# Optimization experiments

Measured on AMD Instinct MI355X. Metric: run time of the kernel, lower is better.

Reference implementation:

```python
import jax, jax.numpy as jnp
import numpy as np

N, E, G = 30000, 480000, 64
IN, H, L = 24, 512, 6


def setup_inputs() -> dict:
    key = jax.random.key(0)
    ks = jax.random.split(key, 20)
    s = 0.05
    inp = {
        "x": jax.random.normal(ks[0], (N, IN), dtype=jnp.float32),
        "edge_index": jax.random.randint(ks[1], (2, E), 0, N, dtype=jnp.int64),
        "batch": jnp.sort(jax.random.randint(ks[2], (N,), 0, G, dtype=jnp.int64)),
        # node encoder
        "enc_w": jax.random.normal(ks[3], (IN, H), dtype=jnp.float32) * s,
        "enc_b": jnp.zeros((H,), dtype=jnp.float32),
        # per-layer message MLP (stacked over L layers), weights stored [in, out]
        "mlp_w1": jax.random.normal(ks[4], (L, H, H), dtype=jnp.float32) * s,
        "mlp_b1": jnp.zeros((L, H), dtype=jnp.float32),
        "mlp_w2": jax.random.normal(ks[5], (L, H, H), dtype=jnp.float32) * s,
        "mlp_b2": jnp.zeros((L, H), dtype=jnp.float32),
        # per-layer GRUCell params, [in, 3H] layout (gates order: r, z, n)
        "gru_wih": jax.random.normal(ks[6], (L, H, 3 * H), dtype=jnp.float32) * s,
        "gru_whh": jax.random.normal(ks[7], (L, H, 3 * H), dtype=jnp.float32) * s,
        "gru_bih": jnp.zeros((L, 3 * H), dtype=jnp.float32),
        "gru_bhh": jnp.zeros((L, 3 * H), dtype=jnp.float32),
        # head MLP
        "head_w1": jax.random.normal(ks[8], (H, H // 2), dtype=jnp.float32) * s,
        "head_b1": jnp.zeros((H // 2,), dtype=jnp.float32),
        "head_w2": jax.random.normal(ks[9], (H // 2, 1), dtype=jnp.float32) * s,
        "head_b2": jnp.zeros((1,), dtype=jnp.float32),
    }
    return inp


def _forward(x, edge_index, batch, enc_w, enc_b, mlp_w1, mlp_b1, mlp_w2, mlp_b2,
             gru_wih, gru_whh, gru_bih, gru_bhh, head_w1, head_b1, head_w2, head_b2):
    src, dst = edge_index[0], edge_index[1]
    h = x @ enc_w + enc_b  # [N, H]
    for l in range(L):
        # message MLP depends only on x_j, so compute per-node then gather
        msg = jnp.maximum(h @ mlp_w1[l] + mlp_b1[l], 0.0) @ mlp_w2[l] + mlp_b2[l]  # [N, H]
        # scatter-add over edges + self-loop contribution (add_self_loops)
        m = jax.ops.segment_sum(msg[src], dst, num_segments=N) + msg  # [N, H]
        # GRUCell(input=m, hidden=h); torch gate order: reset, update, new
        gi = m @ gru_wih[l] + gru_bih[l]
        gh = h @ gru_whh[l] + gru_bhh[l]
        r = jax.nn.sigmoid(gi[:, :H] + gh[:, :H])
        z = jax.nn.sigmoid(gi[:, H:2 * H] + gh[:, H:2 * H])
        n = jnp.tanh(gi[:, 2 * H:] + r * gh[:, 2 * H:])
        h = (1.0 - z) * n + z * h
    # global mean pool per graph
    sums = jax.ops.segment_sum(h, batch, num_segments=G)
    cnt = jax.ops.segment_sum(jnp.ones((N,), dtype=h.dtype), batch, num_segments=G)
    pooled = sums / jnp.maximum(cnt, 1.0)[:, None]  # [G, H]
    out = jnp.maximum(pooled @ head_w1 + head_b1, 0.0) @ head_w2 + head_b2
    return out[:, 0]  # [G]


def reference(x, edge_index, batch, enc_w, enc_b, mlp_w1, mlp_b1, mlp_w2, mlp_b2,
              gru_wih, gru_whh, gru_bih, gru_bhh, head_w1, head_b1, head_w2, head_b2):
    return _forward(x, edge_index, batch, enc_w, enc_b, mlp_w1, mlp_b1, mlp_w2, mlp_b2,
                    gru_wih, gru_whh, gru_bih, gru_bhh, head_w1, head_b1, head_w2, head_b2)
```

## Files before the change

kernel.cpp:

```cpp
#include <hip/hip_runtime.h>
#include <hip/hip_bf16.h>
#include <math.h>

#define N_NODES 30000
#define N_EDGES 480000
#define N_GRAPH 64
#define DIN 24
#define HD 512
#define NL 6

typedef __hip_bfloat16 bf16;
using short8 = __attribute__((ext_vector_type(8))) short;
using f32x4 = __attribute__((ext_vector_type(4))) float;

#define ASYNC16(gp, lp)                                              \
    __builtin_amdgcn_global_load_lds(                                \
        (const __attribute__((address_space(1))) void*)(gp),         \
        (__attribute__((address_space(3))) void*)(lp), 16, 0, 0)

__device__ __forceinline__ float sigmoidf_(float x) { return 1.0f / (1.0f + expf(-x)); }
__device__ __forceinline__ float b2f(unsigned short u) {
    return __uint_as_float(((unsigned int)u) << 16);
}
__device__ __forceinline__ unsigned short f2b(float f) {
    bf16 b = __float2bfloat16(f);
    return *(unsigned short*)&b;
}

__global__ __launch_bounds__(256) void enc_kernel(const float* __restrict__ x,
                                                  const float* __restrict__ w,
                                                  const float* __restrict__ b,
                                                  bf16* __restrict__ h) {
    __shared__ float xs[DIN];
    int row = blockIdx.x;
    int tid = threadIdx.x;
    if (tid < DIN) xs[tid] = x[row * DIN + tid];
    __syncthreads();
    for (int c = tid; c < HD; c += 256) {
        float acc = b[c];
#pragma unroll
        for (int k = 0; k < DIN; k++) acc = fmaf(xs[k], w[k * HD + c], acc);
        h[(size_t)row * HD + c] = __float2bfloat16(acc);
    }
}

__global__ __launch_bounds__(256) void twcvt_kernel(const float* __restrict__ W,
                                                    bf16* __restrict__ WtH,
                                                    bf16* __restrict__ WtL, int Nc) {
    __shared__ float s[32][33];
    int l = blockIdx.z;
    const float* Wp = W + (size_t)l * HD * Nc;
    size_t ob = (size_t)l * HD * Nc;
    int k0 = blockIdx.y * 32, c0 = blockIdx.x * 32;
    int tx = threadIdx.x & 31, ty = threadIdx.x >> 5;
    for (int r = ty; r < 32; r += 8) s[r][tx] = Wp[(size_t)(k0 + r) * Nc + c0 + tx];
    __syncthreads();
    for (int r = ty; r < 32; r += 8) {
        float v = s[tx][r];
        unsigned short hu = f2b(v);
        float hf = b2f(hu);
        size_t o = ob + (size_t)(c0 + r) * HD + k0 + tx;
        *(unsigned short*)&WtH[o] = hu;
        WtL[o] = __float2bfloat16(v - hf);
    }
}

template <bool RELU>
__global__ __launch_bounds__(256) void gemm_mfma(const bf16* __restrict__ A,
                                                 const bf16* __restrict__ WtH,
                                                 const bf16* __restrict__ WtL,
                                                 const float* __restrict__ bias,
                                                 bf16* __restrict__ C, int n) {
    __shared__ bf16 As[128 * 32];
    __shared__ bf16 BH[128 * 32];
    __shared__ bf16 BL[128 * 32];
    int tid = threadIdx.x;
    int wv = tid >> 6, lane = tid & 63;
    int quad = lane >> 4, l16 = lane & 15;
    int crow = lane >> 2, cseg = lane & 3;
    int gseg = cseg ^ ((crow >> 1) & 3);
    int fsw = (quad ^ ((l16 >> 1) & 3)) * 8;
    int row0 = blockIdx.y * 128, col0 = blockIdx.x * 128;
    f32x4 acc[2][8] = {};

    int aoff[4], alds[4];
    int boff[8];
    const bf16* wb = (wv == 2) ? WtH : WtL;
    bf16* bdst = (wv == 2) ? BH : BL;
    if (wv < 2) {
#pragma unroll
        for (int j = 0; j < 4; j++) {
            int ch = wv * 4 + j;
            int gr = row0 + ch * 16 + crow;
            if (gr > n - 1) gr = n - 1;
            aoff[j] = gr * HD + gseg * 8;
            alds[j] = ch * 512;
        }
    } else {
#pragma unroll
        for (int s = 0; s < 8; s++) boff[s] = (col0 + s * 16 + crow) * HD + gseg * 8;
    }

    for (int kt = 0; kt < 512; kt += 32) {
        if (wv < 2) {
#pragma unroll
            for (int j = 0; j < 4; j++) ASYNC16(&A[aoff[j] + kt], &As[alds[j]]);
        } else {
#pragma unroll
            for (int s = 0; s < 8; s++) ASYNC16(&wb[boff[s] + kt], &bdst[s * 512]);
        }
        __syncthreads();
        short8 bhf[2], blf[2];
#pragma unroll
        for (int t = 0; t < 2; t++) {
            int fo = (wv * 32 + t * 16 + l16) * 32 + fsw;
            bhf[t] = *(const short8*)&BH[fo];
            blf[t] = *(const short8*)&BL[fo];
        }
#pragma unroll
        for (int i = 0; i < 8; i++) {
            short8 af = *(const short8*)&As[(i * 16 + l16) * 32 + fsw];
#pragma unroll
            for (int t = 0; t < 2; t++) {
                acc[t][i] = __builtin_amdgcn_mfma_f32_16x16x32_bf16(af, bhf[t], acc[t][i], 0, 0, 0);
                acc[t][i] = __builtin_amdgcn_mfma_f32_16x16x32_bf16(af, blf[t], acc[t][i], 0, 0, 0);
            }
        }
        __syncthreads();
    }
#pragma unroll
    for (int t = 0; t < 2; t++) {
        int col = col0 + wv * 32 + t * 16 + l16;
        float bb = bias[col];
#pragma unroll
        for (int i = 0; i < 8; i++) {
#pragma unroll
            for (int r = 0; r < 4; r++) {
                int row = row0 + i * 16 + quad * 4 + r;
                if (row < n) {
                    float v = acc[t][i][r] + bb;
                    if (RELU) v = fmaxf(v, 0.0f);
                    C[(size_t)row * HD + col] = __float2bfloat16(v);
                }
            }
        }
    }
}

__global__ __launch_bounds__(256, 2) void gru_mfma(const bf16* __restrict__ M,
                                                   const bf16* __restrict__ Hc,
                                                   const bf16* __restrict__ WiH,
                                                   const bf16* __restrict__ WiL,
                                                   const bf16* __restrict__ WhH,
                                                   const bf16* __restrict__ WhL,
                                                   const float* __restrict__ bih,
                                                   const float* __restrict__ bhh,
                                                   bf16* __restrict__ Hn, int n) {
    __shared__ bf16 Ms[128 * 32];
    __shared__ bf16 Hs[128 * 32];
    __shared__ bf16 Ws[12 * 64 * 32];
    int tid = threadIdx.x;
    int wv = tid >> 6, lane = tid & 63;
    int quad = lane >> 4, l16 = lane & 15;
    int crow = lane >> 2, cseg = lane & 3;
    int gseg = cseg ^ ((crow >> 1) & 3);
    int fsw = (quad ^ ((l16 >> 1) & 3)) * 8;
    int row0 = blockIdx.y * 128, col0 = blockIdx.x * 64;
    f32x4 aR[8] = {}, aZ[8] = {}, aI[8] = {}, aHn[8] = {};

    int moff[8];
    const bf16* wgp[4];
    int wlds[4];
    if (wv == 0) {
#pragma unroll
        for (int j = 0; j < 8; j++) {
            int gr = row0 + j * 16 + crow;
            if (gr > n - 1) gr = n - 1;
            moff[j] = gr * HD + gseg * 8;
        }
    } else {
        const bf16* wbase[4] = {WiH, WiL, WhH, WhL};
#pragma unroll
        for (int pp = 0; pp < 4; pp++) {
            int p = (wv - 1) * 4 + pp;
            int mat = (p >= 6);
            int q = p - mat * 6;
            int g = q >> 1, pl = q & 1;
            const bf16* base = wbase[mat * 2 + pl] + (size_t)(g * HD + col0) * HD;
            wgp[pp] = base + crow * HD + gseg * 8;
            wlds[pp] = p * 2048;
        }
    }

    for (int kt = 0; kt < 512; kt += 32) {
        if (wv == 0) {
#pragma unroll
            for (int j = 0; j < 8; j++) {
                ASYNC16(&M[moff[j] + kt], &Ms[j * 512]);
                ASYNC16(&Hc[moff[j] + kt], &Hs[j * 512]);
            }
        } else {
#pragma unroll
            for (int pp = 0; pp < 4; pp++)
#pragma unroll
                for (int s = 0; s < 4; s++)
                    ASYNC16(wgp[pp] + (size_t)s * 16 * HD + kt, &Ws[wlds[pp] + s * 512]);
        }
        __syncthreads();
        short8 wf[12];
        int fo = (wv * 16 + l16) * 32 + fsw;
#pragma unroll
        for (int p = 0; p < 12; p++) wf[p] = *(const short8*)&Ws[p * 2048 + fo];
#pragma unroll
        for (int i = 0; i < 8; i++) {
            int ao = (i * 16 + l16) * 32 + fsw;
            short8 am = *(const short8*)&Ms[ao];
            short8 ah = *(const short8*)&Hs[ao];
            aR[i] = __builtin_amdgcn_mfma_f32_16x16x32_bf16(am, wf[0], aR[i], 0, 0, 0);
            aR[i] = __builtin_amdgcn_mfma_f32_16x16x32_bf16(am, wf[1], aR[i], 0, 0, 0);
            aR[i] = __builtin_amdgcn_mfma_f32_16x16x32_bf16(ah, wf[6], aR[i], 0, 0, 0);
            aR[i] = __builtin_amdgcn_mfma_f32_16x16x32_bf16(ah, wf[7], aR[i], 0, 0, 0);
            aZ[i] = __builtin_amdgcn_mfma_f32_16x16x32_bf16(am, wf[2], aZ[i], 0, 0, 0);
            aZ[i] = __builtin_amdgcn_mfma_f32_16x16x32_bf16(am, wf[3], aZ[i], 0, 0, 0);
            aZ[i] = __builtin_amdgcn_mfma_f32_16x16x32_bf16(ah, wf[8], aZ[i], 0, 0, 0);
            aZ[i] = __builtin_amdgcn_mfma_f32_16x16x32_bf16(ah, wf[9], aZ[i], 0, 0, 0);
            aI[i] = __builtin_amdgcn_mfma_f32_16x16x32_bf16(am, wf[4], aI[i], 0, 0, 0);
            aI[i] = __builtin_amdgcn_mfma_f32_16x16x32_bf16(am, wf[5], aI[i], 0, 0, 0);
            aHn[i] = __builtin_amdgcn_mfma_f32_16x16x32_bf16(ah, wf[10], aHn[i], 0, 0, 0);
            aHn[i] = __builtin_amdgcn_mfma_f32_16x16x32_bf16(ah, wf[11], aHn[i], 0, 0, 0);
        }
        __syncthreads();
    }
    const unsigned short* hp = (const unsigned short*)Hc;
    int col = col0 + wv * 16 + l16;
    float brz = bih[col] + bhh[col];
    float bzz = bih[HD + col] + bhh[HD + col];
    float bin_ = bih[2 * HD + col];
    float bhn_ = bhh[2 * HD + col];
#pragma unroll
    for (int i = 0; i < 8; i++) {
#pragma unroll
        for (int r = 0; r < 4; r++) {
            int row = row0 + i * 16 + quad * 4 + r;
            if (row < n) {
                float rg = sigmoidf_(aR[i][r] + brz);
                float zg = sigmoidf_(aZ[i][r] + bzz);
                float ng = tanhf(aI[i][r] + bin_ + rg * (aHn[i][r] + bhn_));
                float hold = b2f(hp[(size_t)row * HD + col]);
                Hn[(size_t)row * HD + col] = __float2bfloat16((1.0f - zg) * ng + zg * hold);
            }
        }
    }
}

__global__ __launch_bounds__(256) void deg_kernel(const int* __restrict__ dst,
                                                  int* __restrict__ deg) {
    int e = blockIdx.x * 256 + threadIdx.x;
    if (e < N_EDGES) atomicAdd(&deg[dst[e]], 1);
}

__global__ __launch_bounds__(1024) void scan_kernel(const int* __restrict__ deg,
                                                    int* __restrict__ offs) {
    __shared__ int buf[1024];
    __shared__ int carry_s;
    int tid = threadIdx.x;
    if (tid == 0) carry_s = 0;
    __syncthreads();
    for (int base = 0; base < N_NODES; base += 1024) {
        int v = (base + tid < N_NODES) ? deg[base + tid] : 0;
        buf[tid] = v;
        __syncthreads();
        for (int s = 1; s < 1024; s <<= 1) {
            int t = (tid >= s) ? buf[tid - s] : 0;
            __syncthreads();
            buf[tid] += t;
            __syncthreads();
        }
        int incl = buf[tid];
        if (base + tid < N_NODES) offs[base + tid] = carry_s + incl - v;
        __syncthreads();
        if (tid == 0) carry_s += buf[1023];
        __syncthreads();
    }
    if (tid == 0) offs[N_NODES] = carry_s;
}

__global__ __launch_bounds__(256) void bucket_kernel(const int* __restrict__ src,
                                                     const int* __restrict__ dst,
                                                     const int* __restrict__ offs,
                                                     int* __restrict__ cursor,
                                                     unsigned short* __restrict__ elist) {
    int e = blockIdx.x * 256 + threadIdx.x;
    if (e >= N_EDGES) return;
    int d = dst[e];
    int pos = atomicAdd(&cursor[d], 1);
    elist[offs[d] + pos] = (unsigned short)src[e];
}

__global__ __launch_bounds__(256) void gather_kernel(const bf16* __restrict__ msg,
                                                     bf16* __restrict__ m,
                                                     const unsigned short* __restrict__ elist,
                                                     const int* __restrict__ offs) {
    int nid = blockIdx.x, tid = threadIdx.x;
    int beg = offs[nid], end = offs[nid + 1];
    const unsigned int* mp = (const unsigned int*)msg;
    unsigned int u = mp[(size_t)nid * 256 + tid];
    float ax = b2f((unsigned short)(u & 0xffffu));
    float ay = b2f((unsigned short)(u >> 16));
    int e = beg;
    for (; e + 3 < end; e += 4) {
        unsigned int v0 = mp[(size_t)elist[e] * 256 + tid];
        unsigned int v1 = mp[(size_t)elist[e + 1] * 256 + tid];
        unsigned int v2 = mp[(size_t)elist[e + 2] * 256 + tid];
        unsigned int v3 = mp[(size_t)elist[e + 3] * 256 + tid];
        ax += b2f((unsigned short)(v0 & 0xffffu)) + b2f((unsigned short)(v1 & 0xffffu)) +
              b2f((unsigned short)(v2 & 0xffffu)) + b2f((unsigned short)(v3 & 0xffffu));
        ay += b2f((unsigned short)(v0 >> 16)) + b2f((unsigned short)(v1 >> 16)) +
              b2f((unsigned short)(v2 >> 16)) + b2f((unsigned short)(v3 >> 16));
    }
    for (; e < end; e++) {
        unsigned int v0 = mp[(size_t)elist[e] * 256 + tid];
        ax += b2f((unsigned short)(v0 & 0xffffu));
        ay += b2f((unsigned short)(v0 >> 16));
    }
    unsigned int out = ((unsigned int)f2b(ay) << 16) | (unsigned int)f2b(ax);
    ((unsigned int*)m)[(size_t)nid * 256 + tid] = out;
}

__global__ __launch_bounds__(256) void pool_kernel(const bf16* __restrict__ h,
                                                   const int* __restrict__ batch,
                                                   float* __restrict__ pooled,
                                                   float* __restrict__ cnt) {
    int g = blockIdx.x;
    int col = blockIdx.y * 256 + threadIdx.x;
    int lo = 0, hi = N_NODES;
    while (lo < hi) { int mid = (lo + hi) >> 1; if (batch[mid] < g) lo = mid + 1; else hi = mid; }
    int gs = lo;
    hi = N_NODES;
    while (lo < hi) { int mid = (lo + hi) >> 1; if (batch[mid] < g + 1) lo = mid + 1; else hi = mid; }
    int ge = lo;
    const unsigned short* hp = (const unsigned short*)h;
    float acc = 0.0f;
    int r = gs;
    for (; r + 3 < ge; r += 4) {
        acc += b2f(hp[(size_t)r * HD + col]) + b2f(hp[(size_t)(r + 1) * HD + col]) +
               b2f(hp[(size_t)(r + 2) * HD + col]) + b2f(hp[(size_t)(r + 3) * HD + col]);
    }
    for (; r < ge; r++) acc += b2f(hp[(size_t)r * HD + col]);
    pooled[g * HD + col] = acc;
    if (blockIdx.y == 0 && threadIdx.x == 0) cnt[g] = (float)(ge - gs);
}

__global__ __launch_bounds__(256) void head_kernel(const float* __restrict__ pooled,
                                                   const float* __restrict__ cnt,
                                                   const float* __restrict__ w1,
                                                   const float* __restrict__ b1,
                                                   const float* __restrict__ w2,
                                                   const float* __restrict__ b2,
                                                   float* __restrict__ out) {
    __shared__ float prow[HD];
    __shared__ float red[256];
    int g = blockIdx.x, tid = threadIdx.x;
    float c = fmaxf(cnt[g], 1.0f);
    for (int j = tid; j < HD; j += 256) prow[j] = pooled[g * HD + j] / c;
    __syncthreads();
    float acc = b1[tid];
    for (int k = 0; k < HD; k++) acc = fmaf(prow[k], w1[k * 256 + tid], acc);
    red[tid] = fmaxf(acc, 0.0f) * w2[tid];
    __syncthreads();
    for (int s = 128; s > 0; s >>= 1) {
        if (tid < s) red[tid] += red[tid + s];
        __syncthreads();
    }
    if (tid == 0) out[g] = red[0] + b2[0];
}

extern "C" void kernel_launch(void* const* d_in, const int* in_sizes, int n_in,
                              void* d_out, int out_size, void* d_ws, size_t ws_size,
                              hipStream_t stream) {
    const float* x = (const float*)d_in[0];
    const int* eidx = (const int*)d_in[1];
    const int* batch = (const int*)d_in[2];
    const float* enc_w = (const float*)d_in[3];
    const float* enc_b = (const float*)d_in[4];
    const float* mlp_w1 = (const float*)d_in[5];
    const float* mlp_b1 = (const float*)d_in[6];
    const float* mlp_w2 = (const float*)d_in[7];
    const float* mlp_b2 = (const float*)d_in[8];
    const float* gru_wih = (const float*)d_in[9];
    const float* gru_whh = (const float*)d_in[10];
    const float* gru_bih = (const float*)d_in[11];
    const float* gru_bhh = (const float*)d_in[12];
    const float* head_w1 = (const float*)d_in[13];
    const float* head_b1 = (const float*)d_in[14];
    const float* head_w2 = (const float*)d_in[15];
    const float* head_b2 = (const float*)d_in[16];
    const int* src = eidx;
    const int* dst = eidx + N_EDGES;

    const size_t NH = (size_t)N_NODES * HD;
    char* p = (char*)d_ws;
    auto alloc = [&](size_t bytes) { char* q = p; p += (bytes + 255) & ~(size_t)255; return q; };
    bf16* S0 = (bf16*)alloc(NH * 2);
    bf16* S1 = (bf16*)alloc(NH * 2);
    bf16* S2 = (bf16*)alloc(NH * 2);
    bf16* w1tH = (bf16*)alloc((size_t)NL * HD * HD * 2);
    bf16* w1tL = (bf16*)alloc((size_t)NL * HD * HD * 2);
    bf16* w2tH = (bf16*)alloc((size_t)NL * HD * HD * 2);
    bf16* w2tL = (bf16*)alloc((size_t)NL * HD * HD * 2);
    bf16* wihtH = (bf16*)alloc((size_t)NL * 3 * HD * HD * 2);
    bf16* wihtL = (bf16*)alloc((size_t)NL * 3 * HD * HD * 2);
    bf16* whhtH = (bf16*)alloc((size_t)NL * 3 * HD * HD * 2);
    bf16* whhtL = (bf16*)alloc((size_t)NL * 3 * HD * HD * 2);
    float* pooled = (float*)alloc((size_t)N_GRAPH * HD * 4);
    float* cnt = (float*)alloc(N_GRAPH * 4);
    int* deg = (int*)alloc((N_NODES + 1) * 4);
    int* offs = (int*)alloc((N_NODES + 1) * 4);
    unsigned short* elist = (unsigned short*)alloc((size_t)N_EDGES * 2);

    twcvt_kernel<<<dim3(16, 16, NL), 256, 0, stream>>>(mlp_w1, w1tH, w1tL, HD);
    twcvt_kernel<<<dim3(16, 16, NL), 256, 0, stream>>>(mlp_w2, w2tH, w2tL, HD);
    twcvt_kernel<<<dim3(48, 16, NL), 256, 0, stream>>>(gru_wih, wihtH, wihtL, 3 * HD);
    twcvt_kernel<<<dim3(48, 16, NL), 256, 0, stream>>>(gru_whh, whhtH, whhtL, 3 * HD);

    hipMemsetAsync(deg, 0, (N_NODES + 1) * sizeof(int), stream);
    deg_kernel<<<(N_EDGES + 255) / 256, 256, 0, stream>>>(dst, deg);
    scan_kernel<<<1, 1024, 0, stream>>>(deg, offs);
    hipMemsetAsync(deg, 0, (N_NODES + 1) * sizeof(int), stream);
    bucket_kernel<<<(N_EDGES + 255) / 256, 256, 0, stream>>>(src, dst, offs, deg, elist);

    enc_kernel<<<N_NODES, 256, 0, stream>>>(x, enc_w, enc_b, S0);

    bf16* hcur = S0;
    bf16* hoth = S1;
    dim3 ggrid(4, (N_NODES + 127) / 128);
    dim3 ugrid(8, (N_NODES + 127) / 128);

    for (int l = 0; l < NL; l++) {
        size_t wsq = (size_t)l * HD * HD;
        size_t wgq = (size_t)l * 3 * HD * HD;
        const float* b1 = mlp_b1 + (size_t)l * HD;
        const float* b2 = mlp_b2 + (size_t)l * HD;
        const float* bih = gru_bih + (size_t)l * 3 * HD;
        const float* bhh = gru_bhh + (size_t)l * 3 * HD;

        gemm_mfma<true><<<ggrid, 256, 0, stream>>>(hcur, w1tH + wsq, w1tL + wsq, b1, hoth, N_NODES);
        gemm_mfma<false><<<ggrid, 256, 0, stream>>>(hoth, w2tH + wsq, w2tL + wsq, b2, S2, N_NODES);
        gather_kernel<<<N_NODES, 256, 0, stream>>>(S2, hoth, elist, offs);
        gru_mfma<<<ugrid, 256, 0, stream>>>(hoth, hcur, wihtH + wgq, wihtL + wgq,
                                            whhtH + wgq, whhtL + wgq, bih, bhh, S2, N_NODES);
        bf16* newh = S2;
        S2 = hcur;
        hcur = newh;
    }

    pool_kernel<<<dim3(N_GRAPH, 2), 256, 0, stream>>>(hcur, batch, pooled, cnt);
    head_kernel<<<N_GRAPH, 256, 0, stream>>>(pooled, cnt, head_w1, head_b1, head_w2, head_b2,
                                             (float*)d_out);
}
```

Baseline: 2.903 ms.

## Split GRU kernel into r/z and n passes with 8-bit gate staging

Splits the fused GRU GEMM kernel into two kernels. The first computes the r and z gates and stores them quantized to 8 bits each in a scratch buffer. The second computes the n gate and the state update, which roughly halves the accumulators per kernel so launch bounds can target 3 blocks per SM. It also reshapes the MLP GEMM warp tiling so each wave owns 32 rows across all 128 columns instead of 32 columns across all rows. The split re-reads the M and H tiles twice and adds the rz buffer traffic. The 8-bit gate quantization lowers numeric precision.

Result: slower. 3.137 ms (+8.1%).

```diff
diff --git a/kernel.cpp b/kernel.cpp
--- a/kernel.cpp
+++ b/kernel.cpp
@@ -110,35 +110,34 @@
             for (int s = 0; s < 8; s++) ASYNC16(&wb[boff[s] + kt], &bdst[s * 512]);
         }
         __syncthreads();
-        short8 bhf[2], blf[2];
-#pragma unroll
-        for (int t = 0; t < 2; t++) {
-            int fo = (wv * 32 + t * 16 + l16) * 32 + fsw;
-            bhf[t] = *(const short8*)&BH[fo];
-            blf[t] = *(const short8*)&BL[fo];
-        }
-#pragma unroll
-        for (int i = 0; i < 8; i++) {
-            short8 af = *(const short8*)&As[(i * 16 + l16) * 32 + fsw];
-#pragma unroll
-            for (int t = 0; t < 2; t++) {
-                acc[t][i] = __builtin_amdgcn_mfma_f32_16x16x32_bf16(af, bhf[t], acc[t][i], 0, 0, 0);
-                acc[t][i] = __builtin_amdgcn_mfma_f32_16x16x32_bf16(af, blf[t], acc[t][i], 0, 0, 0);
+        short8 af[2];
+#pragma unroll
+        for (int i = 0; i < 2; i++)
+            af[i] = *(const short8*)&As[(wv * 32 + i * 16 + l16) * 32 + fsw];
+#pragma unroll
+        for (int t = 0; t < 8; t++) {
+            int fo = (t * 16 + l16) * 32 + fsw;
+            short8 bh = *(const short8*)&BH[fo];
+            short8 bl = *(const short8*)&BL[fo];
+#pragma unroll
+            for (int i = 0; i < 2; i++) {
+                acc[i][t] = __builtin_amdgcn_mfma_f32_16x16x32_bf16(af[i], bh, acc[i][t], 0, 0, 0);
+                acc[i][t] = __builtin_amdgcn_mfma_f32_16x16x32_bf16(af[i], bl, acc[i][t], 0, 0, 0);
             }
         }
         __syncthreads();
     }
 #pragma unroll
-    for (int t = 0; t < 2; t++) {
-        int col = col0 + wv * 32 + t * 16 + l16;
+    for (int t = 0; t < 8; t++) {
+        int col = col0 + t * 16 + l16;
         float bb = bias[col];
 #pragma unroll
-        for (int i = 0; i < 8; i++) {
+        for (int i = 0; i < 2; i++) {
 #pragma unroll
             for (int r = 0; r < 4; r++) {
-                int row = row0 + i * 16 + quad * 4 + r;
+                int row = row0 + wv * 32 + i * 16 + quad * 4 + r;
                 if (row < n) {
-                    float v = acc[t][i][r] + bb;
+                    float v = acc[i][t][r] + bb;
                     if (RELU) v = fmaxf(v, 0.0f);
                     C[(size_t)row * HD + col] = __float2bfloat16(v);
                 }
@@ -147,18 +146,18 @@
     }
 }
 
-__global__ __launch_bounds__(256, 2) void gru_mfma(const bf16* __restrict__ M,
-                                                   const bf16* __restrict__ Hc,
-                                                   const bf16* __restrict__ WiH,
-                                                   const bf16* __restrict__ WiL,
-                                                   const bf16* __restrict__ WhH,
-                                                   const bf16* __restrict__ WhL,
-                                                   const float* __restrict__ bih,
-                                                   const float* __restrict__ bhh,
-                                                   bf16* __restrict__ Hn, int n) {
+__global__ __launch_bounds__(256, 3) void gruA(const bf16* __restrict__ M,
+                                               const bf16* __restrict__ Hc,
+                                               const bf16* __restrict__ WiH,
+                                               const bf16* __restrict__ WiL,
+                                               const bf16* __restrict__ WhH,
+                                               const bf16* __restrict__ WhL,
+                                               const float* __restrict__ bih,
+                                               const float* __restrict__ bhh,
+                                               unsigned short* __restrict__ rz, int n) {
     __shared__ bf16 Ms[128 * 32];
     __shared__ bf16 Hs[128 * 32];
-    __shared__ bf16 Ws[12 * 64 * 32];
+    __shared__ bf16 Ws[8 * 64 * 32];
     int tid = threadIdx.x;
     int wv = tid >> 6, lane = tid & 63;
     int quad = lane >> 4, l16 = lane & 15;
@@ -166,12 +165,12 @@
     int gseg = cseg ^ ((crow >> 1) & 3);
     int fsw = (quad ^ ((l16 >> 1) & 3)) * 8;
     int row0 = blockIdx.y * 128, col0 = blockIdx.x * 64;
-    f32x4 aR[8] = {}, aZ[8] = {}, aI[8] = {}, aHn[8] = {};
+    f32x4 aR[8] = {}, aZ[8] = {};
 
     int moff[8];
     const bf16* wgp[4];
     int wlds[4];
-    if (wv == 0) {
+    if (wv < 2) {
 #pragma unroll
         for (int j = 0; j < 8; j++) {
             int gr = row0 + j * 16 + crow;
@@ -179,14 +178,13 @@
             moff[j] = gr * HD + gseg * 8;
         }
     } else {
-        const bf16* wbase[4] = {WiH, WiL, WhH, WhL};
 #pragma unroll
         for (int pp = 0; pp < 4; pp++) {
-            int p = (wv - 1) * 4 + pp;
-            int mat = (p >= 6);
-            int q = p - mat * 6;
-            int g = q >> 1, pl = q & 1;
-            const bf16* base = wbase[mat * 2 + pl] + (size_t)(g * HD + col0) * HD;
+            int p = (wv - 2) * 4 + pp;
+            int g = (p >> 1) & 1;
+            int pl = p & 1;
+            const bf16* base = (p < 4) ? (pl ? WiL : WiH) : (pl ? WhL : WhH);
+            base += (size_t)(g * HD + col0) * HD;
             wgp[pp] = base + crow * HD + gseg * 8;
             wlds[pp] = p * 2048;
         }
@@ -195,10 +193,10 @@
     for (int kt = 0; kt < 512; kt += 32) {
         if (wv == 0) {
 #pragma unroll
-            for (int j = 0; j < 8; j++) {
-                ASYNC16(&M[moff[j] + kt], &Ms[j * 512]);
-                ASYNC16(&Hc[moff[j] + kt], &Hs[j * 512]);
-            }
+            for (int j = 0; j < 8; j++) ASYNC16(&M[moff[j] + kt], &Ms[j * 512]);
+        } else if (wv == 1) {
+#pragma unroll
+            for (int j = 0; j < 8; j++) ASYNC16(&Hc[moff[j] + kt], &Hs[j * 512]);
         } else {
 #pragma unroll
             for (int pp = 0; pp < 4; pp++)
@@ -207,10 +205,10 @@
                     ASYNC16(wgp[pp] + (size_t)s * 16 * HD + kt, &Ws[wlds[pp] + s * 512]);
         }
         __syncthreads();
-        short8 wf[12];
+        short8 wf[8];
         int fo = (wv * 16 + l16) * 32 + fsw;
 #pragma unroll
-        for (int p = 0; p < 12; p++) wf[p] = *(const short8*)&Ws[p * 2048 + fo];
+        for (int p = 0; p < 8; p++) wf[p] = *(const short8*)&Ws[p * 2048 + fo];
 #pragma unroll
         for (int i = 0; i < 8; i++) {
             int ao = (i * 16 + l16) * 32 + fsw;
@@ -218,25 +216,18 @@
             short8 ah = *(const short8*)&Hs[ao];
             aR[i] = __builtin_amdgcn_mfma_f32_16x16x32_bf16(am, wf[0], aR[i], 0, 0, 0);
             aR[i] = __builtin_amdgcn_mfma_f32_16x16x32_bf16(am, wf[1], aR[i], 0, 0, 0);
-            aR[i] = __builtin_amdgcn_mfma_f32_16x16x32_bf16(ah, wf[6], aR[i], 0, 0, 0);
-            aR[i] = __builtin_amdgcn_mfma_f32_16x16x32_bf16(ah, wf[7], aR[i], 0, 0, 0);
+            aR[i] = __builtin_amdgcn_mfma_f32_16x16x32_bf16(ah, wf[4], aR[i], 0, 0, 0);
+            aR[i] = __builtin_amdgcn_mfma_f32_16x16x32_bf16(ah, wf[5], aR[i], 0, 0, 0);
             aZ[i] = __builtin_amdgcn_mfma_f32_16x16x32_bf16(am, wf[2], aZ[i], 0, 0, 0);
             aZ[i] = __builtin_amdgcn_mfma_f32_16x16x32_bf16(am, wf[3], aZ[i], 0, 0, 0);
-            aZ[i] = __builtin_amdgcn_mfma_f32_16x16x32_bf16(ah, wf[8], aZ[i], 0, 0, 0);
-            aZ[i] = __builtin_amdgcn_mfma_f32_16x16x32_bf16(ah, wf[9], aZ[i], 0, 0, 0);
-            aI[i] = __builtin_amdgcn_mfma_f32_16x16x32_bf16(am, wf[4], aI[i], 0, 0, 0);
-            aI[i] = __builtin_amdgcn_mfma_f32_16x16x32_bf16(am, wf[5], aI[i], 0, 0, 0);
-            aHn[i] = __builtin_amdgcn_mfma_f32_16x16x32_bf16(ah, wf[10], aHn[i], 0, 0, 0);
-            aHn[i] = __builtin_amdgcn_mfma_f32_16x16x32_bf16(ah, wf[11], aHn[i], 0, 0, 0);
-        }
-        __syncthreads();
-    }
-    const unsigned short* hp = (const unsigned short*)Hc;
+            aZ[i] = __builtin_amdgcn_mfma_f32_16x16x32_bf16(ah, wf[6], aZ[i], 0, 0, 0);
+            aZ[i] = __builtin_amdgcn_mfma_f32_16x16x32_bf16(ah, wf[7], aZ[i], 0, 0, 0);
+        }
+        __syncthreads();
+    }
     int col = col0 + wv * 16 + l16;
     float brz = bih[col] + bhh[col];
     float bzz = bih[HD + col] + bhh[HD + col];
-    float bin_ = bih[2 * HD + col];
-    float bhn_ = bhh[2 * HD + col];
 #pragma unroll
     for (int i = 0; i < 8; i++) {
 #pragma unroll
@@ -245,6 +236,103 @@
             if (row < n) {
                 float rg = sigmoidf_(aR[i][r] + brz);
                 float zg = sigmoidf_(aZ[i][r] + bzz);
+                unsigned int qr = (unsigned int)(rg * 255.0f + 0.5f);
+                unsigned int qz = (unsigned int)(zg * 255.0f + 0.5f);
+                rz[(size_t)row * HD + col] = (unsigned short)(qr | (qz << 8));
+            }
+        }
+    }
+}
+
+__global__ __launch_bounds__(256, 3) void gruB(const bf16* __restrict__ M,
+                                               const bf16* __restrict__ Hc,
+                                               const bf16* __restrict__ WiH,
+                                               const bf16* __restrict__ WiL,
+                                               const bf16* __restrict__ WhH,
+                                               const bf16* __restrict__ WhL,
+                                               const float* __restrict__ bih,
+                                               const float* __restrict__ bhh,
+                                               const unsigned short* __restrict__ rz,
+                                               bf16* __restrict__ Hn, int n) {
+    __shared__ bf16 Ms[128 * 32];
+    __shared__ bf16 Hs[128 * 32];
+    __shared__ bf16 Ws[4 * 64 * 32];
+    int tid = threadIdx.x;
+    int wv = tid >> 6, lane = tid & 63;
+    int quad = lane >> 4, l16 = lane & 15;
+    int crow = lane >> 2, cseg = lane & 3;
+    int gseg = cseg ^ ((crow >> 1) & 3);
+    int fsw = (quad ^ ((l16 >> 1) & 3)) * 8;
+    int row0 = blockIdx.y * 128, col0 = blockIdx.x * 64;
+    f32x4 aI[8] = {}, aHn[8] = {};
+
+    int moff[8];
+    const bf16* wgp[2];
+    int wlds[2];
+    if (wv < 2) {
+#pragma unroll
+        for (int j = 0; j < 8; j++) {
+            int gr = row0 + j * 16 + crow;
+            if (gr > n - 1) gr = n - 1;
+            moff[j] = gr * HD + gseg * 8;
+        }
+    } else {
+#pragma unroll
+        for (int pp = 0; pp < 2; pp++) {
+            int p = (wv - 2) * 2 + pp;
+            int pl = p & 1;
+            const bf16* base = (p < 2) ? (pl ? WiL : WiH) : (pl ? WhL : WhH);
+            base += (size_t)(2 * HD + col0) * HD;
+            wgp[pp] = base + crow * HD + gseg * 8;
+            wlds[pp] = p * 2048;
+        }
+    }
+
+    for (int kt = 0; kt < 512; kt += 32) {
+        if (wv == 0) {
+#pragma unroll
+            for (int j = 0; j < 8; j++) ASYNC16(&M[moff[j] + kt], &Ms[j * 512]);
+        } else if (wv == 1) {
+#pragma unroll
+            for (int j = 0; j < 8; j++) ASYNC16(&Hc[moff[j] + kt], &Hs[j * 512]);
+        } else {
+#pragma unroll
+            for (int pp = 0; pp < 2; pp++)
+#pragma unroll
+                for (int s = 0; s < 4; s++)
+                    ASYNC16(wgp[pp] + (size_t)s * 16 * HD + kt, &Ws[wlds[pp] + s * 512]);
+        }
+        __syncthreads();
+        short8 wf[4];
+        int fo = (wv * 16 + l16) * 32 + fsw;
+#pragma unroll
+        for (int p = 0; p < 4; p++) wf[p] = *(const short8*)&Ws[p * 2048 + fo];
+#pragma unroll
+        for (int i = 0; i < 8; i++) {
+            int ao = (i * 16 + l16) * 32 + fsw;
+            short8 am = *(const short8*)&Ms[ao];
+            short8 ah = *(const short8*)&Hs[ao];
+            aI[i] = __builtin_amdgcn_mfma_f32_16x16x32_bf16(am, wf[0], aI[i], 0, 0, 0);
+            aI[i] = __builtin_amdgcn_mfma_f32_16x16x32_bf16(am, wf[1], aI[i], 0, 0, 0);
+            aHn[i] = __builtin_amdgcn_mfma_f32_16x16x32_bf16(ah, wf[2], aHn[i], 0, 0, 0);
+            aHn[i] = __builtin_amdgcn_mfma_f32_16x16x32_bf16(ah, wf[3], aHn[i], 0, 0, 0);
+        }
+        __syncthreads();
+    }
+    const unsigned short* hp = (const unsigned short*)Hc;
+    int col = col0 + wv * 16 + l16;
+    float bin_ = bih[2 * HD + col];
+    float bhn_ = bhh[2 * HD + col];
+    const float inv255 = 1.0f / 255.0f;
+#pragma unroll
+    for (int i = 0; i < 8; i++) {
+#pragma unroll
+        for (int r = 0; r < 4; r++) {
+            int row = row0 + i * 16 + quad * 4 + r;
+            if (row < n) {
+                unsigned short q = rz[(size_t)row * HD + col];
+                float rg = (float)(q & 255) * inv255;
+                float zg = (float)(q >> 8) * inv255;
                 float ng = tanhf(aI[i][r] + bin_ + rg * (aHn[i][r] + bhn_));
                 float hold = b2f(hp[(size_t)row * HD + col]);
                 Hn[(size_t)row * HD + col] = __float2bfloat16((1.0f - zg) * ng + zg * hold);
@@ -404,6 +492,7 @@
     bf16* S0 = (bf16*)alloc(NH * 2);
     bf16* S1 = (bf16*)alloc(NH * 2);
     bf16* S2 = (bf16*)alloc(NH * 2);
+    unsigned short* rzbuf = (unsigned short*)alloc(NH * 2);
     bf16* w1tH = (bf16*)alloc((size_t)NL * HD * HD * 2);
     bf16* w1tL = (bf16*)alloc((size_t)NL * HD * HD * 2);
     bf16* w2tH = (bf16*)alloc((size_t)NL * HD * HD * 2);
@@ -447,8 +536,10 @@
         gemm_mfma<true><<<ggrid, 256, 0, stream>>>(hcur, w1tH + wsq, w1tL + wsq, b1, hoth, N_NODES);
         gemm_mfma<false><<<ggrid, 256, 0, stream>>>(hoth, w2tH + wsq, w2tL + wsq, b2, S2, N_NODES);
         gather_kernel<<<N_NODES, 256, 0, stream>>>(S2, hoth, elist, offs);
-        gru_mfma<<<ugrid, 256, 0, stream>>>(hoth, hcur, wihtH + wgq, wihtL + wgq,
-                                            whhtH + wgq, whhtL + wgq, bih, bhh, S2, N_NODES);
+        gruA<<<ugrid, 256, 0, stream>>>(hoth, hcur, wihtH + wgq, wihtL + wgq,
+                                        whhtH + wgq, whhtL + wgq, bih, bhh, rzbuf, N_NODES);
+        gruB<<<ugrid, 256, 0, stream>>>(hoth, hcur, wihtH + wgq, wihtL + wgq,
+                                        whhtH + wgq, whhtL + wgq, bih, bhh, rzbuf, S2, N_NODES);
         bf16* newh = S2;
         S2 = hcur;
         hcur = newh;
```
